# Kernel tuning notes

Measured on AMD Instinct MI355X. Metric: run time of the kernel, lower is better.

Reference implementation:

```python
import jax, jax.numpy as jnp
from jax import lax
import numpy as np

B = 16384
D = 32
N_HEADS = 4


def _piece_table():
    base = np.zeros((7, 4, 4), np.int32)
    cells = [
        [(1, 0), (1, 1), (1, 2), (1, 3)],  # I
        [(1, 1), (1, 2), (2, 1), (2, 2)],  # O
        [(1, 1), (2, 0), (2, 1), (2, 2)],  # T
        [(1, 1), (1, 2), (2, 0), (2, 1)],  # S
        [(1, 0), (1, 1), (2, 1), (2, 2)],  # Z
        [(1, 0), (2, 0), (2, 1), (2, 2)],  # J
        [(1, 2), (2, 0), (2, 1), (2, 2)],  # L
    ]
    for i, cs in enumerate(cells):
        for (r, c) in cs:
            base[i, r, c] = 1
    rots = np.stack([np.stack([np.rot90(base[i], k) for k in range(4)]) for i in range(7)])
    p = np.concatenate([rots, np.zeros((1, 4, 4, 4), np.int32)], 0)  # [8,4,4,4]
    return jnp.asarray(p)


def setup_inputs() -> dict:
    key = jax.random.key(0)
    ks = jax.random.split(key, 24)

    def ri(k, n, lo, hi):
        return jax.random.randint(k, (B, n), lo, hi, dtype=jnp.int32)

    t = jnp.concatenate([
        ri(ks[0], 1, 0, 10),   # col0 feature
        ri(ks[1], 1, 2, 8),
        ri(ks[2], 1, 0, 10),   # col2 y pos
        ri(ks[3], 1, 0, 8),    # col3 drop dist
        ri(ks[4], 1, 0, 4),    # col4 rotation
        ri(ks[5], 3, 0, 10),   # cols5-7
        ri(ks[6], 1, 0, 7),    # col8 piece id
        ri(ks[7], 6, 0, 7),    # cols9-14 hold/next
        ri(ks[8], 7, 0, 10),   # cols15-21
        ri(ks[9], 210, 0, 2),  # cols22-231 board
    ], axis=1)

    s = 0.05
    rn = lambda k, shp: jax.random.normal(k, shp, jnp.float32) * s
    return {
        "t": t,
        "piece_table": _piece_table(),
        "conv1_w": rn(ks[10], (6, 3, 5, 5)), "conv1_b": rn(ks[11], (6,)),
        "conv2_w": rn(ks[12], (16, 6, 5, 5)), "conv2_b": rn(ks[13], (16,)),
        "conv3_w": rn(ks[14], (64, 16, 3, 1)), "conv3_b": rn(ks[15], (64,)),
        "lfc1_w": rn(ks[16], (32, 64)), "lfc1_b": rn(ks[17], (32,)),
        "fc_w": rn(ks[18], (32, 8)), "fc_b": rn(ks[19], (32,)),
        "emb": rn(ks[20], (8, D)),
        "in_proj_w": rn(ks[21], (3 * D, D)), "in_proj_b": jnp.zeros((3 * D,), jnp.float32),
        "out_proj_w": rn(ks[22], (D, D)), "out_proj_b": jnp.zeros((D,), jnp.float32),
    }


def _avgpool2(x):
    b, c, h, w = x.shape
    h2, w2 = h // 2, w // 2
    return x[:, :, :h2 * 2, :w2 * 2].reshape(b, c, h2, 2, w2, 2).mean((3, 5))


def _lenet(x, w1, b1, w2, b2, w3, b3, fw, fb):
    dn = ("NCHW", "OIHW", "NCHW")
    x = jax.nn.relu(lax.conv_general_dilated(x, w1, (1, 1), ((2, 2), (2, 2)), dimension_numbers=dn) + b1[None, :, None, None])
    x = _avgpool2(x)                                   # [B,6,11,6]
    x = jax.nn.relu(lax.conv_general_dilated(x, w2, (1, 1), ((0, 0), (0, 0)), dimension_numbers=dn) + b2[None, :, None, None])
    x = _avgpool2(x)                                   # [B,16,3,1]
    x = jax.nn.relu(lax.conv_general_dilated(x, w3, (1, 1), ((0, 0), (0, 0)), dimension_numbers=dn) + b3[None, :, None, None])
    x = x.reshape(-1, 64)
    return jax.nn.relu(x @ fw.T + fb)                  # [B,32]


def _pe():
    pos = jnp.array([0, 0, 1, 2, 3, 4, 5], jnp.float32)[:, None]
    div = jnp.exp(jnp.arange(0, D, 2, dtype=jnp.float32) * (-jnp.log(10000.0) / D))
    s, c = jnp.sin(pos * div), jnp.cos(pos * div)      # [7,16] each
    return jnp.stack([s, c], -1).reshape(7, D)         # interleaved sin/cos


def _mha(q_in, kv, in_w, in_b, out_w, out_b):
    qw, kw, vw = in_w[:D], in_w[D:2 * D], in_w[2 * D:]
    qb, kb, vb = in_b[:D], in_b[D:2 * D], in_b[2 * D:]
    b, lq, _ = q_in.shape
    hd = D // N_HEADS
    q = (q_in @ qw.T + qb).reshape(b, lq, N_HEADS, hd)
    k = (kv @ kw.T + kb).reshape(b, -1, N_HEADS, hd)
    v = (kv @ vw.T + vb).reshape(b, -1, N_HEADS, hd)
    scores = jnp.einsum("bqhd,bkhd->bhqk", q, k) / jnp.sqrt(jnp.float32(hd))
    w = jax.nn.softmax(scores, axis=-1)
    o = jnp.einsum("bhqk,bkhd->bqhd", w, v).reshape(b, lq, D)
    return o @ out_w.T + out_b


def reference(t, piece_table, conv1_w, conv1_b, conv2_w, conv2_b, conv3_w, conv3_b,
              lfc1_w, lfc1_b, fc_w, fc_b, emb, in_proj_w, in_proj_b, out_proj_w, out_proj_b):
    bsz = t.shape[0]
    board = jnp.zeros((bsz, 3, 21, 10), jnp.float32)
    board = board.at[:, 0].set(t[:, 22:232].astype(jnp.float32).reshape(bsz, 21, 10))

    # gather piece grid, extract the 4 filled cells per sample in row-major order
    pieces = piece_table[t[:, 8], t[:, 4]].reshape(bsz, 16)        # [B,16] in {0,1}
    idx = jnp.argsort(1 - pieces, axis=1, stable=True)[:, :4]      # first 4 ones, scan order
    cy, cx = idx // 4, idx % 4
    x = cx + t[:, 1][:, None] - 2
    y = cy + t[:, 2][:, None]
    ny = y + t[:, 3][:, None]
    mask = (y >= 0) & (ny >= 0)
    br = jnp.arange(bsz, dtype=jnp.int32)[:, None]
    y_m = jnp.where(mask, y, -1)
    ny_m = jnp.where(mask, ny, -1)
    board = board.at[br, 1, y_m, x].set(1.0, mode="drop")
    board = board.at[br, 2, ny_m, x].set(1.0, mode="drop")

    board = jnp.pad(board, ((0, 0), (0, 0), (0, 1), (1, 1)), constant_values=1.0)  # [B,3,22,12]

    t9 = jnp.where((t[:, 9] != -1) & (t[:, 6] != 0), t[:, 9], 7)
    hold_next = jnp.concatenate([t[:, 8:9], t9[:, None], t[:, 10:15]], axis=1)     # [B,7]

    b2 = _lenet(board, conv1_w, conv1_b, conv2_w, conv2_b, conv3_w, conv3_b, lfc1_w, lfc1_b)  # [B,32]
    bkv = b2[:, None, :]                                            # [B,1,32]
    p = emb[hold_next] + _pe()[None]                                # [B,7,32]
    a = _mha(p, bkv, in_proj_w, in_proj_b, out_proj_w, out_proj_b)  # [B,7,32]

    xf = jax.nn.relu(t[:, :8].astype(jnp.float32) @ fc_w.T + fc_b)  # [B,32]
    out = jnp.concatenate([xf, a.mean(axis=1), b2], axis=1)         # [B,96]
    return (out, board)
```

## Files before the change

kernel.cpp:

```cpp
#include <hip/hip_runtime.h>
#include <cstddef>


#define BATCH 16384
#define SPB   4
#define NBLK  (BATCH / SPB)
#define RS    18
#define SS2   884

__global__ __launch_bounds__(256)
void cborder_kernel(const float* __restrict__ w1, float* __restrict__ cb)
{
  int i = blockIdx.x * 256 + threadIdx.x;
  if (i >= 1584) return;
  int p = i / 6, o = i - p * 6;
  int y0 = p / 12, x0 = p - y0 * 12;
  float acc = 0.f;
#pragma unroll
  for (int dy = 0; dy < 5; ++dy)
#pragma unroll
    for (int dx = 0; dx < 5; ++dx) {
      int pr = y0 + dy - 2, pc = x0 + dx - 2;
      if (pr >= 0 && pr < 22 && pc >= 0 && pc < 12 &&
          (pr == 21 || pc == 0 || pc == 11)) {
        int k = dy * 5 + dx;
        acc += w1[(o * 3 + 0) * 25 + k] + w1[(o * 3 + 1) * 25 + k]
             + w1[(o * 3 + 2) * 25 + k];
      }
    }
  cb[p * 6 + o] = acc;
}

__global__ __launch_bounds__(256)
void board_model_kernel(const int* __restrict__ t,
                        const int* __restrict__ piece_table,
                        const float* __restrict__ w1, const float* __restrict__ b1,
                        const float* __restrict__ w2, const float* __restrict__ b2w,
                        const float* __restrict__ w3, const float* __restrict__ b3,
                        const float* __restrict__ wf1, const float* __restrict__ bf1,
                        const float* __restrict__ fcw, const float* __restrict__ fcb,
                        const float* __restrict__ ipw, const float* __restrict__ ipb,
                        const float* __restrict__ opw, const float* __restrict__ opb,
                        const float* __restrict__ cbg,
                        float* __restrict__ out,
                        float* __restrict__ out_board)
{
  __shared__ __align__(16) float scr[SPB * SS2];
  __shared__ float w1L[450];
  __shared__ float cbL[1584];

  const int tid  = threadIdx.x;
  const int lane = tid & 63;
  const int wv   = tid >> 6;
  const int bb   = blockIdx.x * SPB;

  for (int i = tid; i < 450; i += 256) w1L[i] = w1[i];
  for (int i = tid; i < 1584; i += 256) cbL[i] = cbg[i];

  {
    float* W = &scr[wv * SS2];
    int*   pcs = (int*)&scr[wv * SS2 + 864];
    const int* tr = t + (size_t)(bb + wv) * 232;

    float4* W4 = (float4*)W;
    for (int i = lane; i < 117; i += 64) W4[i] = float4{0.f, 0.f, 0.f, 0.f};

    for (int i = lane; i < 210; i += 64) {
      int r = i / 10, b = i - r * 10;
      W[(r + 2) * RS + b + 5] = (float)tr[22 + i];
    }

    if (lane < 4) {
      const int* pt = piece_table + (tr[8] * 4 + tr[4]) * 16;
      int sel = -1, n1 = 0;
#pragma unroll
      for (int j = 0; j < 16; ++j) { if (pt[j]) { if (n1 == lane) sel = j; ++n1; } }
      if (sel < 0) {
        int n0 = 0, want = lane - n1;
#pragma unroll
        for (int j = 0; j < 16; ++j) if (!pt[j]) { if (n0 == want) { sel = j; break; } ++n0; }
      }
      int cy = sel >> 2, cx = sel & 3;
      int x  = cx + tr[1] - 2;
      int y  = cy + tr[2];
      int ny = y + tr[3];
      bool mask = (y >= 0) && (ny >= 0);
      bool xok  = (x >= 0) && (x < 10);
      bool v1 = mask && xok && (y < 21);
      bool v2 = mask && xok && (ny < 21);
      pcs[2 * lane + 0]       = v1 ? y  : -100;
      pcs[2 * lane + 1]       = x + 1;
      pcs[2 * (lane + 4)]     = v2 ? ny : -100;
      pcs[2 * (lane + 4) + 1] = x + 1;
    }
    __builtin_amdgcn_wave_barrier();

    float* ob = out_board + (size_t)(bb + wv) * 792;
    for (int v = lane; v < 198; v += 64) {
      int j0 = v * 4;
      int ch = j0 / 264, rem = j0 - ch * 264;
      int r = rem / 12, c = rem - r * 12;
      float val[4];
      if (ch == 0) {
#pragma unroll
        for (int d = 0; d < 4; ++d) {
          int cd = c + d;
          val[d] = (r == 21 || cd == 0 || cd == 11) ? 1.f
                 : W[(r + 2) * RS + cd + 4];
        }
      } else {
#pragma unroll
        for (int d = 0; d < 4; ++d) {
          int cd = c + d;
          val[d] = (r == 21 || cd == 0 || cd == 11) ? 1.f : 0.f;
        }
#pragma unroll
        for (int e = 0; e < 4; ++e) {
          int pr = pcs[2 * ((ch - 1) * 4 + e)];
          int pc = pcs[2 * ((ch - 1) * 4 + e) + 1];
          if (pr == r && (unsigned)(pc - c) < 4u) val[pc - c] = 1.f;
        }
      }
      *(float4*)(ob + j0) = float4{val[0], val[1], val[2], val[3]};
    }
  }
  __syncthreads();

  {
    int g = tid;
    int q = g / 66, p = g - q * 66;
    int r = p / 6, c = p - r * 6;
    const float* Wq  = &scr[q * SS2];
    const int*   pcs = (const int*)&scr[q * SS2 + 864];
    float acc[2][2][6];
#pragma unroll
    for (int i = 0; i < 2; ++i)
#pragma unroll
      for (int j = 0; j < 2; ++j) {
        int pcell = (2 * r + i) * 12 + (2 * c + j);
#pragma unroll
        for (int o = 0; o < 6; ++o)
          acc[i][j][o] = b1[o] + cbL[pcell * 6 + o];
      }

    {
      const float* base = Wq + (2 * r) * RS + (2 * c + 2);
#pragma unroll
      for (int u = 0; u < 6; ++u) {
        float2 a0 = *(const float2*)(base + u * RS);
        float2 a1 = *(const float2*)(base + u * RS + 2);
        float2 a2 = *(const float2*)(base + u * RS + 4);
        float rv[6] = {a0.x, a0.y, a1.x, a1.y, a2.x, a2.y};
#pragma unroll
        for (int i = 0; i < 2; ++i) {
          if (u - i < 0 || u - i > 4) continue;
          const int ky = u - i;
#pragma unroll
          for (int j = 0; j < 2; ++j)
#pragma unroll
            for (int kx = 0; kx < 5; ++kx) {
              float xv = rv[j + kx];
#pragma unroll
              for (int o = 0; o < 6; ++o)
                acc[i][j][o] += xv * w1[o * 75 + ky * 5 + kx];
            }
        }
      }
    }

#pragma unroll
    for (int e = 0; e < 8; ++e) {
      int pr = pcs[2 * e];
      if (pr < 0) continue;
      int pc = pcs[2 * e + 1];
      int ch = 1 + (e >> 2);
      int dyb = pr + 2 - 2 * r;
      int dxb = pc + 2 - 2 * c;
      if (dyb < 0 || dyb > 5 || dxb < 0 || dxb > 5) continue;
#pragma unroll
      for (int i = 0; i < 2; ++i) {
        int dy = dyb - i;
        if ((unsigned)dy >= 5u) continue;
#pragma unroll
        for (int j = 0; j < 2; ++j) {
          int dx = dxb - j;
          if ((unsigned)dx >= 5u) continue;
#pragma unroll
          for (int o = 0; o < 6; ++o)
            acc[i][j][o] += w1L[o * 75 + ch * 25 + dy * 5 + dx];
        }
      }
    }

    float* P1q = &scr[q * SS2 + 468];
#pragma unroll
    for (int o = 0; o < 6; ++o) {
      float v = fmaxf(acc[0][0][o], 0.f) + fmaxf(acc[0][1][o], 0.f)
              + fmaxf(acc[1][0][o], 0.f) + fmaxf(acc[1][1][o], 0.f);
      P1q[o * 66 + p] = 0.25f * v;
    }
  }

  {
    const int g16 = lane >> 4;
    const int kl  = lane & 15;
    const float* W3b  = &scr[3 * SS2];
    const int*   pcs3 = (const int*)&scr[3 * SS2 + 864];
    float psum[6] = {0.f, 0.f, 0.f, 0.f, 0.f, 0.f};
#pragma unroll
    for (int cc2 = 0; cc2 < 2; ++cc2) {
      int cell = (wv * 4 + g16) * 2 + cc2;
      int pos  = 58 + (cell >> 2);
      int sub  = cell & 3;
      int rp = pos / 6, cp = pos - rp * 6;
      int y0 = 2 * rp + (sub >> 1), x0 = 2 * cp + (sub & 1);
      float a6[6] = {0.f, 0.f, 0.f, 0.f, 0.f, 0.f};
#pragma unroll
      for (int it = 0; it < 2; ++it) {
        int k = kl + 16 * it;
        if (k < 25) {
          int dy = k / 5, dx = k - dy * 5;
          float xv = W3b[(y0 + dy) * RS + x0 + dx + 2];
#pragma unroll
          for (int o = 0; o < 6; ++o)
            a6[o] += xv * w1L[o * 75 + dy * 5 + dx];
        }
      }
#pragma unroll
      for (int o = 0; o < 6; ++o) {
        float v = a6[o];
        v += __shfl_xor(v, 1, 64);  v += __shfl_xor(v, 2, 64);
        v += __shfl_xor(v, 4, 64);  v += __shfl_xor(v, 8, 64);
        a6[o] = v + b1[o] + cbL[(y0 * 12 + x0) * 6 + o];
      }
#pragma unroll
      for (int e = 0; e < 8; ++e) {
        int pr = pcs3[2 * e];
        if (pr < 0) continue;
        int pc = pcs3[2 * e + 1];
        int ch = 1 + (e >> 2);
        int dy = pr + 2 - y0;
        int dx = pc + 2 - x0;
        if ((unsigned)dy < 5u && (unsigned)dx < 5u) {
#pragma unroll
          for (int o = 0; o < 6; ++o)
            a6[o] += w1L[o * 75 + ch * 25 + dy * 5 + dx];
        }
      }
#pragma unroll
      for (int o = 0; o < 6; ++o) psum[o] += fmaxf(a6[o], 0.f);
    }
#pragma unroll
    for (int o = 0; o < 6; ++o)
      psum[o] += __shfl_xor(psum[o], 16, 64);
    if (kl == 0 && (g16 & 1) == 0) {
      int pos = 58 + wv * 2 + (g16 >> 1);
#pragma unroll
      for (int o = 0; o < 6; ++o)
        scr[3 * SS2 + 468 + o * 66 + pos] = 0.25f * psum[o];
    }
  }
  __syncthreads();

  const int wvu = __builtin_amdgcn_readfirstlane(wv);

  if (lane < 48) {
    int q = lane / 12, p = lane - q * 12;
    int r = p >> 1, c = p & 1;
    const float* P1q = &scr[q * SS2 + 468];
    float a4[4];
#pragma unroll
    for (int oo = 0; oo < 4; ++oo) a4[oo] = b2w[4 * wvu + oo];
    for (int ic = 0; ic < 6; ++ic)
#pragma unroll
      for (int kr = 0; kr < 5; ++kr) {
        float xv[5];
#pragma unroll
        for (int kc = 0; kc < 5; ++kc)
          xv[kc] = P1q[ic * 66 + (r + kr) * 6 + c + kc];
#pragma unroll
        for (int kc = 0; kc < 5; ++kc)
#pragma unroll
          for (int oo = 0; oo < 4; ++oo)
            a4[oo] += xv[kc] * w2[(((4 * wvu + oo) * 6 + ic) * 5 + kr) * 5 + kc];
      }
    float* C2q = &scr[q * SS2];
#pragma unroll
    for (int oo = 0; oo < 4; ++oo)
      C2q[(4 * wvu + oo) * 12 + p] = fmaxf(a4[oo], 0.f);
  }
  __syncthreads();

  {
    const int q = wvu;
    float* S = &scr[q * SS2];

    if (lane < 48) {
      int o = lane / 3, pr = lane - o * 3;
      float v = 0.25f * (S[o * 12 + 4 * pr] + S[o * 12 + 4 * pr + 1]
                       + S[o * 12 + 4 * pr + 2] + S[o * 12 + 4 * pr + 3]);
      S[192 + lane] = v;
    }
    __builtin_amdgcn_wave_barrier();

    {
      int o = lane;
      float acc = b3[o];
#pragma unroll
      for (int k = 0; k < 48; ++k) acc += S[192 + k] * w3[o * 48 + k];
      S[240 + o] = fmaxf(acc, 0.f);
    }
    __builtin_amdgcn_wave_barrier();

    {
      int j = lane & 31, h = lane >> 5;
      float part = 0.f;
#pragma unroll
      for (int kk = 0; kk < 32; ++kk) {
        int k = 32 * h + kk;
        part += S[240 + k] * wf1[j * 64 + k];
      }
      part += __shfl_xor(part, 32, 64);
      if (h == 0) {
        float acc = fmaxf(bf1[j] + part, 0.f);
        S[304 + j] = acc;
        out[(size_t)(bb + q) * 96 + 64 + j] = acc;
      }
    }
    __builtin_amdgcn_wave_barrier();

    {
      int j = lane & 31;
      if (lane < 32) {
        float acc = ipb[64 + j];
#pragma unroll
        for (int k = 0; k < 32; ++k) acc += S[304 + k] * ipw[(64 + j) * 32 + k];
        S[336 + j] = acc;
      } else {
        const int* tr = t + (size_t)(bb + q) * 232;
        float acc = fcb[j];
#pragma unroll
        for (int k = 0; k < 8; ++k) acc += (float)tr[k] * fcw[j * 8 + k];
        out[(size_t)(bb + q) * 96 + j] = fmaxf(acc, 0.f);
      }
    }
    __builtin_amdgcn_wave_barrier();

    if (lane < 32) {
      int j = lane;
      float acc = opb[j];
#pragma unroll
      for (int k = 0; k < 32; ++k) acc += S[336 + k] * opw[j * 32 + k];
      out[(size_t)(bb + q) * 96 + 32 + j] = acc;
    }
  }
}

extern "C" void kernel_launch(void* const* d_in, const int* in_sizes, int n_in,
                              void* d_out, int out_size, void* d_ws, size_t ws_size,
                              hipStream_t stream) {
  const int*   t   = (const int*)d_in[0];
  const int*   pt  = (const int*)d_in[1];
  const float* w1  = (const float*)d_in[2];
  const float* b1  = (const float*)d_in[3];
  const float* w2  = (const float*)d_in[4];
  const float* b2w = (const float*)d_in[5];
  const float* w3  = (const float*)d_in[6];
  const float* b3  = (const float*)d_in[7];
  const float* wf1 = (const float*)d_in[8];
  const float* bf1 = (const float*)d_in[9];
  const float* fcw = (const float*)d_in[10];
  const float* fcb = (const float*)d_in[11];
  const float* ipw = (const float*)d_in[13];
  const float* ipb = (const float*)d_in[14];
  const float* opw = (const float*)d_in[15];
  const float* opb = (const float*)d_in[16];

  float* out       = (float*)d_out;
  float* out_board = out + (size_t)BATCH * 96;
  float* cbg       = (float*)d_ws;

  hipLaunchKernelGGL(cborder_kernel, dim3(7), dim3(256), 0, stream, w1, cbg);
  hipLaunchKernelGGL(board_model_kernel, dim3(NBLK), dim3(256), 0, stream,
                     t, pt, w1, b1, w2, b2w, w3, b3, wf1, bf1, fcw, fcb,
                     ipw, ipb, opw, opb, cbg, out, out_board);
}
```

Baseline: 212.7 us.

## Drop unused bottom pooled row from conv1 and compact shared-memory layout

Conv1+pool now computes only the 60 pooled positions that conv2 actually reads, dropping the 11th pooled row. That removes the extra cross-wave pass that covered the remaining positions with shuffle reductions. Each wave now handles its own sample's 60 outputs, and the per-sample scratch, w1 cache (only channels 1-2 kept) and border table shrink to match. This cuts work and LDS footprint but leaves 4 of 64 lanes idle in the conv1 stage and depends on the index arithmetic staying consistent.

Result: faster. 196.3 us (-7.7%).

```diff
diff --git a/kernel.cpp b/kernel.cpp
--- a/kernel.cpp
+++ b/kernel.cpp
@@ -6,7 +6,10 @@
 #define SPB   4
 #define NBLK  (BATCH / SPB)
 #define RS    18
-#define SS2   884
+#define SBE_SZ 432
+#define P1OFF  432
+#define PCSOFF 800
+#define SS2    816
 
 __global__ __launch_bounds__(256)
 void cborder_kernel(const float* __restrict__ w1, float* __restrict__ cb)
@@ -46,24 +49,25 @@
                         float* __restrict__ out_board)
 {
   __shared__ __align__(16) float scr[SPB * SS2];
-  __shared__ float w1L[450];
-  __shared__ float cbL[1584];
+  __shared__ float w1L[300];
+  __shared__ float cbL[1440];
 
   const int tid  = threadIdx.x;
   const int lane = tid & 63;
   const int wv   = tid >> 6;
   const int bb   = blockIdx.x * SPB;
 
-  for (int i = tid; i < 450; i += 256) w1L[i] = w1[i];
-  for (int i = tid; i < 1584; i += 256) cbL[i] = cbg[i];
+  for (int i = tid; i < 300; i += 256)
+    w1L[i] = w1[(i / 50) * 75 + 25 + (i % 50)];
+  for (int i = tid; i < 1440; i += 256) cbL[i] = cbg[i];
 
   {
     float* W = &scr[wv * SS2];
-    int*   pcs = (int*)&scr[wv * SS2 + 864];
+    int*   pcs = (int*)&scr[wv * SS2 + PCSOFF];
     const int* tr = t + (size_t)(bb + wv) * 232;
 
     float4* W4 = (float4*)W;
-    for (int i = lane; i < 117; i += 64) W4[i] = float4{0.f, 0.f, 0.f, 0.f};
+    for (int i = lane; i < 108; i += 64) W4[i] = float4{0.f, 0.f, 0.f, 0.f};
 
     for (int i = lane; i < 210; i += 64) {
       int r = i / 10, b = i - r * 10;
@@ -126,12 +130,11 @@
   }
   __syncthreads();
 
-  {
-    int g = tid;
-    int q = g / 66, p = g - q * 66;
+  if (lane < 60) {
+    int p = lane;
     int r = p / 6, c = p - r * 6;
-    const float* Wq  = &scr[q * SS2];
-    const int*   pcs = (const int*)&scr[q * SS2 + 864];
+    const float* Wq  = &scr[wv * SS2];
+    const int*   pcs = (const int*)&scr[wv * SS2 + PCSOFF];
     float acc[2][2][6];
 #pragma unroll
     for (int i = 0; i < 2; ++i)
@@ -173,7 +176,7 @@
       int pr = pcs[2 * e];
       if (pr < 0) continue;
       int pc = pcs[2 * e + 1];
-      int ch = 1 + (e >> 2);
+      int chm = e >> 2;
       int dyb = pr + 2 - 2 * r;
       int dxb = pc + 2 - 2 * c;
       if (dyb < 0 || dyb > 5 || dxb < 0 || dxb > 5) continue;
@@ -187,77 +190,17 @@
           if ((unsigned)dx >= 5u) continue;
 #pragma unroll
           for (int o = 0; o < 6; ++o)
-            acc[i][j][o] += w1L[o * 75 + ch * 25 + dy * 5 + dx];
-        }
-      }
-    }
-
-    float* P1q = &scr[q * SS2 + 468];
+            acc[i][j][o] += w1L[(o * 2 + chm) * 25 + dy * 5 + dx];
+        }
+      }
+    }
+
+    float* P1q = &scr[wv * SS2 + P1OFF];
 #pragma unroll
     for (int o = 0; o < 6; ++o) {
       float v = fmaxf(acc[0][0][o], 0.f) + fmaxf(acc[0][1][o], 0.f)
               + fmaxf(acc[1][0][o], 0.f) + fmaxf(acc[1][1][o], 0.f);
-      P1q[o * 66 + p] = 0.25f * v;
-    }
-  }
-
-  {
-    const int g16 = lane >> 4;
-    const int kl  = lane & 15;
-    const float* W3b  = &scr[3 * SS2];
-    const int*   pcs3 = (const int*)&scr[3 * SS2 + 864];
-    float psum[6] = {0.f, 0.f, 0.f, 0.f, 0.f, 0.f};
-#pragma unroll
-    for (int cc2 = 0; cc2 < 2; ++cc2) {
-      int cell = (wv * 4 + g16) * 2 + cc2;
-      int pos  = 58 + (cell >> 2);
-      int sub  = cell & 3;
-      int rp = pos / 6, cp = pos - rp * 6;
-      int y0 = 2 * rp + (sub >> 1), x0 = 2 * cp + (sub & 1);
-      float a6[6] = {0.f, 0.f, 0.f, 0.f, 0.f, 0.f};
-#pragma unroll
-      for (int it = 0; it < 2; ++it) {
-        int k = kl + 16 * it;
-        if (k < 25) {
-          int dy = k / 5, dx = k - dy * 5;
-          float xv = W3b[(y0 + dy) * RS + x0 + dx + 2];
-#pragma unroll
-          for (int o = 0; o < 6; ++o)
-            a6[o] += xv * w1L[o * 75 + dy * 5 + dx];
-        }
-      }
-#pragma unroll
-      for (int o = 0; o < 6; ++o) {
-        float v = a6[o];
-        v += __shfl_xor(v, 1, 64);  v += __shfl_xor(v, 2, 64);
-        v += __shfl_xor(v, 4, 64);  v += __shfl_xor(v, 8, 64);
-        a6[o] = v + b1[o] + cbL[(y0 * 12 + x0) * 6 + o];
-      }
-#pragma unroll
-      for (int e = 0; e < 8; ++e) {
-        int pr = pcs3[2 * e];
-        if (pr < 0) continue;
-        int pc = pcs3[2 * e + 1];
-        int ch = 1 + (e >> 2);
-        int dy = pr + 2 - y0;
-        int dx = pc + 2 - x0;
-        if ((unsigned)dy < 5u && (unsigned)dx < 5u) {
-#pragma unroll
-          for (int o = 0; o < 6; ++o)
-            a6[o] += w1L[o * 75 + ch * 25 + dy * 5 + dx];
-        }
-      }
-#pragma unroll
-      for (int o = 0; o < 6; ++o) psum[o] += fmaxf(a6[o], 0.f);
-    }
-#pragma unroll
-    for (int o = 0; o < 6; ++o)
-      psum[o] += __shfl_xor(psum[o], 16, 64);
-    if (kl == 0 && (g16 & 1) == 0) {
-      int pos = 58 + wv * 2 + (g16 >> 1);
-#pragma unroll
-      for (int o = 0; o < 6; ++o)
-        scr[3 * SS2 + 468 + o * 66 + pos] = 0.25f * psum[o];
+      P1q[o * 61 + p] = 0.25f * v;
     }
   }
   __syncthreads();
@@ -267,7 +210,7 @@
   if (lane < 48) {
     int q = lane / 12, p = lane - q * 12;
     int r = p >> 1, c = p & 1;
-    const float* P1q = &scr[q * SS2 + 468];
+    const float* P1q = &scr[q * SS2 + P1OFF];
     float a4[4];
 #pragma unroll
     for (int oo = 0; oo < 4; ++oo) a4[oo] = b2w[4 * wvu + oo];
@@ -277,7 +220,7 @@
         float xv[5];
 #pragma unroll
         for (int kc = 0; kc < 5; ++kc)
-          xv[kc] = P1q[ic * 66 + (r + kr) * 6 + c + kc];
+          xv[kc] = P1q[ic * 61 + (r + kr) * 6 + c + kc];
 #pragma unroll
         for (int kc = 0; kc < 5; ++kc)
 #pragma unroll
```
